# Kernel tuning notes

Hardware: AMD Instinct MI355X
Metric: run time of the kernel (lower is better)

Reference implementation:

```python
import jax, jax.numpy as jnp
import numpy as np

N_ROWS = 4096   # output features (N)
M_COLS = 4096   # input features (M)
BATCH = 4096
NNZ_PER_ROW = 819


def setup_inputs() -> dict:
    rng = np.random.default_rng(0)
    # sample NNZ_PER_ROW distinct, sorted column indices per row (CSR structure)
    cols = np.argsort(rng.random((N_ROWS, M_COLS)), axis=1)[:, :NNZ_PER_ROW]
    cols = np.sort(cols, axis=1).reshape(-1).astype(np.int32)            # [nnz]
    row_ids = np.repeat(np.arange(N_ROWS, dtype=np.int32), NNZ_PER_ROW)  # [nnz], expanded indptr

    key = jax.random.key(0)
    k1, k2, k3 = jax.random.split(key, 3)
    inp = jax.random.normal(k1, (BATCH, M_COLS), dtype=jnp.float32)
    W_val = jax.random.normal(k2, (N_ROWS * NNZ_PER_ROW,), dtype=jnp.float32) * 0.02
    bias = jax.random.normal(k3, (N_ROWS,), dtype=jnp.float32)
    return {
        "input": inp,
        "W_val": W_val,
        "bias": bias,
        "row_ids": jnp.asarray(row_ids),
        "cols": jnp.asarray(cols),
        "N": N_ROWS,
    }


def reference(input, W_val, bias, row_ids, cols, N):
    # Faithful math of SparseLinearFunction: y = x @ W^T + bias where W is the
    # CSR matrix (W_val, row_ids, cols) of shape (N, M). Densify via scatter
    # (CSR has unique (row, col) pairs) then use a single GEMM.
    M = input.shape[-1]
    W = jnp.zeros((N, M), dtype=W_val.dtype).at[row_ids, cols].set(W_val)  # [N, M]
    return jnp.matmul(input, W.T) + bias  # [B, N]
```

## Files before the change

### kernel.cpp

```cpp
#include <hip/hip_runtime.h>
#include <hip/hip_bf16.h>
#include <stdint.h>


#define B_DIM 4096
#define M_DIM 4096
#define N_DIM 4096
#define NNZ_ROW 819
#define BK 32

typedef __attribute__((ext_vector_type(8))) __bf16 bf16x8;
typedef __attribute__((ext_vector_type(4))) float f32x4;

__device__ __forceinline__ unsigned short f32_to_bf16(float f) {
    union { float f; unsigned int u; } v;
    v.f = f;
    unsigned int r = v.u + 0x7FFFu + ((v.u >> 16) & 1u);
    return (unsigned short)(r >> 16);
}

__device__ __forceinline__ void load_lds16(const void* g, void* l) {
    __builtin_amdgcn_global_load_lds(
        (const __attribute__((address_space(1))) void*)g,
        (__attribute__((address_space(3))) void*)l,
        16, 0, 0);
}

__global__ __launch_bounds__(256) void densify_w(
    const float* __restrict__ wval,
    const int* __restrict__ cols,
    unsigned short* __restrict__ wb) {
    __shared__ __attribute__((aligned(16))) unsigned short row_s[M_DIM];
    const int row = blockIdx.x;
    const int tid = threadIdx.x;
    uint4* rs4 = (uint4*)row_s;
    rs4[tid]       = make_uint4(0u, 0u, 0u, 0u);
    rs4[tid + 256] = make_uint4(0u, 0u, 0u, 0u);
    __syncthreads();
    const size_t base = (size_t)row * NNZ_ROW;
    for (int j = tid; j < NNZ_ROW; j += 256) {
        const int c = cols[base + j];
        row_s[c] = f32_to_bf16(wval[base + j]);
    }
    __syncthreads();
    uint4* dst = (uint4*)(wb + (size_t)row * M_DIM);
    dst[tid]       = rs4[tid];
    dst[tid + 256] = rs4[tid + 256];
}

__global__ __launch_bounds__(256) void cvt_x_bf16(
    const float4* __restrict__ x, uint4* __restrict__ y, int n8) {
    int i = blockIdx.x * 256 + threadIdx.x;
    if (i >= n8) return;
    const float4 a = x[2 * i];
    const float4 b = x[2 * i + 1];
    union { ushort ush[8]; uint4 u4; } o;
    o.ush[0] = f32_to_bf16(a.x); o.ush[1] = f32_to_bf16(a.y);
    o.ush[2] = f32_to_bf16(a.z); o.ush[3] = f32_to_bf16(a.w);
    o.ush[4] = f32_to_bf16(b.x); o.ush[5] = f32_to_bf16(b.y);
    o.ush[6] = f32_to_bf16(b.z); o.ush[7] = f32_to_bf16(b.w);
    y[i] = o.u4;
}


__global__ __launch_bounds__(256, 4) void gemm_bt_bias(
    const unsigned short* __restrict__ Xb,
    const unsigned short* __restrict__ Wb,
    const float* __restrict__ bias,
    float* __restrict__ out)
{
    __shared__ __attribute__((aligned(16))) unsigned short As[2 * 128 * BK];
    __shared__ __attribute__((aligned(16))) unsigned short Bs[2 * 128 * BK];

    const int tid    = threadIdx.x;
    const int wid    = tid >> 6;
    const int lane   = tid & 63;
    const int wm     = wid & 1;
    const int wn     = wid >> 1;
    const int lane15 = lane & 15;
    const int laneq  = lane >> 4;

    const int bm0 = blockIdx.y * 128;
    const int bn0 = blockIdx.x * 128;

    const int srow = (lane >> 2);
    const int skof = ((lane & 3) ^ ((lane >> 3) & 3)) * 8;

    const unsigned short* aSrc0 =
        Xb + (size_t)(bm0 + wid * 16 + srow) * M_DIM + skof;
    const unsigned short* aSrc1 = aSrc0 + (size_t)64 * M_DIM;
    const unsigned short* bSrc0 =
        Wb + (size_t)(bn0 + wid * 16 + srow) * M_DIM + skof;
    const unsigned short* bSrc1 = bSrc0 + (size_t)64 * M_DIM;

    const int dOff0 = wid * 512;
    const int dOff1 = (wid + 4) * 512;

    const int slot = (laneq ^ ((lane15 >> 1) & 3)) * 8;
    int aOff[4], bOff[4];
#pragma unroll
    for (int t = 0; t < 4; ++t) {
        aOff[t] = (wm * 64 + t * 16 + lane15) * BK + slot;
        bOff[t] = (wn * 64 + t * 16 + lane15) * BK + slot;
    }

    f32x4 acc[4][4];
#pragma unroll
    for (int i = 0; i < 4; ++i)
#pragma unroll
        for (int j = 0; j < 4; ++j) acc[i][j] = (f32x4)0.0f;

    load_lds16(aSrc0, As + dOff0);
    load_lds16(aSrc1, As + dOff1);
    load_lds16(bSrc0, Bs + dOff0);
    load_lds16(bSrc1, Bs + dOff1);
    __syncthreads();

    int buf = 0;
    for (int kt = 0; kt < M_DIM; kt += BK) {
        const int nbase = (buf ^ 1) * (128 * BK);
        if (kt + BK < M_DIM) {
            load_lds16(aSrc0 + kt + BK, As + nbase + dOff0);
            load_lds16(aSrc1 + kt + BK, As + nbase + dOff1);
            load_lds16(bSrc0 + kt + BK, Bs + nbase + dOff0);
            load_lds16(bSrc1 + kt + BK, Bs + nbase + dOff1);
        }
        const int cbase = buf * (128 * BK);

        bf16x8 af[4], bf[4];
#pragma unroll
        for (int t = 0; t < 4; ++t) {
            af[t] = *((const bf16x8*)(As + cbase + aOff[t]));
            bf[t] = *((const bf16x8*)(Bs + cbase + bOff[t]));
        }
#pragma unroll
        for (int mt = 0; mt < 4; ++mt)
#pragma unroll
            for (int nt = 0; nt < 4; ++nt)
                acc[mt][nt] = __builtin_amdgcn_mfma_f32_16x16x32_bf16(
                    af[mt], bf[nt], acc[mt][nt], 0, 0, 0);

        __syncthreads();
        buf ^= 1;
    }

#pragma unroll
    for (int nt = 0; nt < 4; ++nt) {
        const int col = bn0 + wn * 64 + nt * 16 + lane15;
        const float bv = bias[col];
#pragma unroll
        for (int mt = 0; mt < 4; ++mt) {
            const int row0 = bm0 + wm * 64 + mt * 16 + laneq * 4;
#pragma unroll
            for (int r = 0; r < 4; ++r) {
                out[(size_t)(row0 + r) * N_DIM + col] = acc[mt][nt][r] + bv;
            }
        }
    }
}


extern "C" void kernel_launch(void* const* d_in, const int* in_sizes, int n_in,
                              void* d_out, int out_size, void* d_ws, size_t ws_size,
                              hipStream_t stream) {
    const float* x       = (const float*)d_in[0];
    const float* wval    = (const float*)d_in[1];
    const float* bias    = (const float*)d_in[2];
    const int*   cols    = (const int*)d_in[4];
    float* out = (float*)d_out;

    unsigned short* Wb = (unsigned short*)d_ws;
    unsigned short* Xb = Wb + (size_t)N_DIM * M_DIM;

    densify_w<<<dim3(N_DIM), dim3(256), 0, stream>>>(wval, cols, Wb);
    {
        int n8 = (B_DIM * M_DIM) / 8;
        cvt_x_bf16<<<dim3(n8 / 256), dim3(256), 0, stream>>>(
            (const float4*)x, (uint4*)Xb, n8);
    }
    gemm_bt_bias<<<dim3(N_DIM / 128, B_DIM / 128), dim3(256), 0, stream>>>(
        Xb, Wb, bias, out);
}
```

Before: 296.9 us.

## Rewrite GEMM as 256x256 tile, 8-wave, BK=64 phased pipeline with XCD swizzle

Replaces the 128x128, 4-wave, BK=32 double-buffered GEMM with a 256x256 block tile computed by 8 waves. Each 64-wide K step is split into four quadrant phases that interleave global-to-LDS staging with MFMA work, using a manual vmcnt wait and raw barriers plus setprio around the MFMA clusters. Block indices are also remapped so that neighbouring tiles land on the same XCD for L2 reuse. The aim is more data reuse per LDS load and better overlap of loads with compute. The cost is higher register and LDS use (128KB shared) and hand-tuned wait counts, which are fragile.

```diff
diff --git a/kernel.cpp b/kernel.cpp
--- a/kernel.cpp
+++ b/kernel.cpp
@@ -7,7 +7,6 @@
 #define M_DIM 4096
 #define N_DIM 4096
 #define NNZ_ROW 819
-#define BK 32
 
 typedef __attribute__((ext_vector_type(8))) __bf16 bf16x8;
 typedef __attribute__((ext_vector_type(4))) float f32x4;
@@ -62,101 +61,147 @@
     y[i] = o.u4;
 }
 
-
-__global__ __launch_bounds__(256, 4) void gemm_bt_bias(
+__device__ __forceinline__ void stage_half(
+    const unsigned short* __restrict__ src,
+    int grow0,
+    int kt,
+    unsigned short* dst,
+    int w, int l) {
+#pragma unroll
+    for (int j = 0; j < 2; ++j) {
+        const int seg = w * 2 + j;
+        const int r   = seg * 8 + (l >> 3);
+        const int cg  = (l >> 3) ^ (l & 7);
+        load_lds16(src + (size_t)(grow0 + r) * M_DIM + kt + cg * 8,
+                   dst + seg * 512);
+    }
+}
+
+template <int MA, int NB, int SK>
+__device__ __forceinline__ void phase_op(
+    const unsigned short* As_c, const unsigned short* Bs_c,
+    unsigned short* As_n, unsigned short* Bs_n,
+    const unsigned short* __restrict__ Xb, const unsigned short* __restrict__ Wb,
+    int bm0, int bn0, int kn, bool do_stage,
+    int wr, int wc, int w, int l, f32x4 (&acc)[2][4][2][2]) {
+    const int l15 = l & 15;
+    const int lg  = l >> 4;
+    const int lx  = l & 7;
+    const int ck0 = (lg ^ lx) << 3;
+    const int ck1 = ((4 + lg) ^ lx) << 3;
+
+    const unsigned short* Ab = As_c + (MA * 128 + wr * 64 + l15) * 64;
+    const unsigned short* Bb = Bs_c + (NB * 128 + wc * 32 + l15) * 64;
+
+    bf16x8 af[4][2], bfr[2][2];
+#pragma unroll
+    for (int mf = 0; mf < 4; ++mf) {
+        af[mf][0] = *(const bf16x8*)(Ab + mf * 1024 + ck0);
+        af[mf][1] = *(const bf16x8*)(Ab + mf * 1024 + ck1);
+    }
+#pragma unroll
+    for (int nf = 0; nf < 2; ++nf) {
+        bfr[nf][0] = *(const bf16x8*)(Bb + nf * 1024 + ck0);
+        bfr[nf][1] = *(const bf16x8*)(Bb + nf * 1024 + ck1);
+    }
+
+    if (do_stage) {
+        if constexpr (SK == 0) stage_half(Xb, bm0,       kn, As_n,        w, l);
+        if constexpr (SK == 1) stage_half(Wb, bn0,       kn, Bs_n,        w, l);
+        if constexpr (SK == 2) stage_half(Xb, bm0 + 128, kn, As_n + 8192, w, l);
+        if constexpr (SK == 3) stage_half(Wb, bn0 + 128, kn, Bs_n + 8192, w, l);
+    }
+
+    asm volatile("s_waitcnt vmcnt(4)" ::: "memory");
+    asm volatile("s_barrier" ::: "memory");
+
+    __builtin_amdgcn_s_setprio(1);
+#pragma unroll
+    for (int mf = 0; mf < 4; ++mf)
+#pragma unroll
+        for (int nf = 0; nf < 2; ++nf) {
+            acc[MA][mf][NB][nf] = __builtin_amdgcn_mfma_f32_16x16x32_bf16(
+                af[mf][0], bfr[nf][0], acc[MA][mf][NB][nf], 0, 0, 0);
+            acc[MA][mf][NB][nf] = __builtin_amdgcn_mfma_f32_16x16x32_bf16(
+                af[mf][1], bfr[nf][1], acc[MA][mf][NB][nf], 0, 0, 0);
+        }
+    __builtin_amdgcn_s_setprio(0);
+    asm volatile("s_barrier" ::: "memory");
+}
+
+__global__ __launch_bounds__(512, 2) void gemm_bt_bias(
     const unsigned short* __restrict__ Xb,
     const unsigned short* __restrict__ Wb,
     const float* __restrict__ bias,
     float* __restrict__ out)
 {
-    __shared__ __attribute__((aligned(16))) unsigned short As[2 * 128 * BK];
-    __shared__ __attribute__((aligned(16))) unsigned short Bs[2 * 128 * BK];
-
-    const int tid    = threadIdx.x;
-    const int wid    = tid >> 6;
-    const int lane   = tid & 63;
-    const int wm     = wid & 1;
-    const int wn     = wid >> 1;
-    const int lane15 = lane & 15;
-    const int laneq  = lane >> 4;
-
-    const int bm0 = blockIdx.y * 128;
-    const int bn0 = blockIdx.x * 128;
-
-    const int srow = (lane >> 2);
-    const int skof = ((lane & 3) ^ ((lane >> 3) & 3)) * 8;
-
-    const unsigned short* aSrc0 =
-        Xb + (size_t)(bm0 + wid * 16 + srow) * M_DIM + skof;
-    const unsigned short* aSrc1 = aSrc0 + (size_t)64 * M_DIM;
-    const unsigned short* bSrc0 =
-        Wb + (size_t)(bn0 + wid * 16 + srow) * M_DIM + skof;
-    const unsigned short* bSrc1 = bSrc0 + (size_t)64 * M_DIM;
-
-    const int dOff0 = wid * 512;
-    const int dOff1 = (wid + 4) * 512;
-
-    const int slot = (laneq ^ ((lane15 >> 1) & 3)) * 8;
-    int aOff[4], bOff[4];
-#pragma unroll
-    for (int t = 0; t < 4; ++t) {
-        aOff[t] = (wm * 64 + t * 16 + lane15) * BK + slot;
-        bOff[t] = (wn * 64 + t * 16 + lane15) * BK + slot;
-    }
-
-    f32x4 acc[4][4];
-#pragma unroll
-    for (int i = 0; i < 4; ++i)
-#pragma unroll
-        for (int j = 0; j < 4; ++j) acc[i][j] = (f32x4)0.0f;
-
-    load_lds16(aSrc0, As + dOff0);
-    load_lds16(aSrc1, As + dOff1);
-    load_lds16(bSrc0, Bs + dOff0);
-    load_lds16(bSrc1, Bs + dOff1);
-    __syncthreads();
-
-    int buf = 0;
-    for (int kt = 0; kt < M_DIM; kt += BK) {
-        const int nbase = (buf ^ 1) * (128 * BK);
-        if (kt + BK < M_DIM) {
-            load_lds16(aSrc0 + kt + BK, As + nbase + dOff0);
-            load_lds16(aSrc1 + kt + BK, As + nbase + dOff1);
-            load_lds16(bSrc0 + kt + BK, Bs + nbase + dOff0);
-            load_lds16(bSrc1 + kt + BK, Bs + nbase + dOff1);
+    __shared__ __attribute__((aligned(16))) unsigned short As0[16384];
+    __shared__ __attribute__((aligned(16))) unsigned short Bs0[16384];
+    __shared__ __attribute__((aligned(16))) unsigned short As1[16384];
+    __shared__ __attribute__((aligned(16))) unsigned short Bs1[16384];
+
+    const int tid = threadIdx.x;
+    const int w   = tid >> 6;
+    const int l   = tid & 63;
+    const int wr  = w >> 2;
+    const int wc  = w & 3;
+
+    const int wg  = blockIdx.y * 16 + blockIdx.x;
+    const int idx = ((wg & 7) << 5) | (wg >> 3);
+    const int bm0 = (idx >> 4) * 256;
+    const int bn0 = (idx & 15) * 256;
+
+    f32x4 acc[2][4][2][2];
+#pragma unroll
+    for (int a = 0; a < 2; ++a)
+#pragma unroll
+        for (int b = 0; b < 4; ++b)
+#pragma unroll
+            for (int c = 0; c < 2; ++c)
+#pragma unroll
+                for (int d = 0; d < 2; ++d) acc[a][b][c][d] = (f32x4)0.0f;
+
+    stage_half(Xb, bm0,       0, As0,        w, l);
+    stage_half(Wb, bn0,       0, Bs0,        w, l);
+    stage_half(Xb, bm0 + 128, 0, As0 + 8192, w, l);
+    stage_half(Wb, bn0 + 128, 0, Bs0 + 8192, w, l);
+    asm volatile("s_waitcnt vmcnt(0)" ::: "memory");
+    asm volatile("s_barrier" ::: "memory");
+
+#pragma unroll 1
+    for (int kt = 0; kt < M_DIM; kt += 128) {
+        const int k1 = kt + 64;
+        const int k2 = kt + 128;
+        const bool s2 = (k2 < M_DIM);
+        phase_op<0,0,0>(As0,Bs0, As1,Bs1, Xb,Wb, bm0,bn0, k1, true, wr,wc,w,l, acc);
+        phase_op<1,0,1>(As0,Bs0, As1,Bs1, Xb,Wb, bm0,bn0, k1, true, wr,wc,w,l, acc);
+        phase_op<1,1,2>(As0,Bs0, As1,Bs1, Xb,Wb, bm0,bn0, k1, true, wr,wc,w,l, acc);
+        phase_op<0,1,3>(As0,Bs0, As1,Bs1, Xb,Wb, bm0,bn0, k1, true, wr,wc,w,l, acc);
+        phase_op<0,0,0>(As1,Bs1, As0,Bs0, Xb,Wb, bm0,bn0, k2, s2,   wr,wc,w,l, acc);
+        phase_op<1,0,1>(As1,Bs1, As0,Bs0, Xb,Wb, bm0,bn0, k2, s2,   wr,wc,w,l, acc);
+        phase_op<1,1,2>(As1,Bs1, As0,Bs0, Xb,Wb, bm0,bn0, k2, s2,   wr,wc,w,l, acc);
+        phase_op<0,1,3>(As1,Bs1, As0,Bs0, Xb,Wb, bm0,bn0, k2, s2,   wr,wc,w,l, acc);
+    }
+
+    const int l15 = l & 15;
+    const int lg  = l >> 4;
+#pragma unroll
+    for (int nb = 0; nb < 2; ++nb)
+#pragma unroll
+        for (int nf = 0; nf < 2; ++nf) {
+            const int col = bn0 + nb * 128 + wc * 32 + nf * 16 + l15;
+            const float bv = bias[col];
+#pragma unroll
+            for (int ma = 0; ma < 2; ++ma)
+#pragma unroll
+                for (int mf = 0; mf < 4; ++mf) {
+                    const int row0 = bm0 + ma * 128 + wr * 64 + mf * 16 + lg * 4;
+#pragma unroll
+                    for (int r = 0; r < 4; ++r)
+                        out[(size_t)(row0 + r) * N_DIM + col] =
+                            acc[ma][mf][nb][nf][r] + bv;
+                }
         }
-        const int cbase = buf * (128 * BK);
-
-        bf16x8 af[4], bf[4];
-#pragma unroll
-        for (int t = 0; t < 4; ++t) {
-            af[t] = *((const bf16x8*)(As + cbase + aOff[t]));
-            bf[t] = *((const bf16x8*)(Bs + cbase + bOff[t]));
-        }
-#pragma unroll
-        for (int mt = 0; mt < 4; ++mt)
-#pragma unroll
-            for (int nt = 0; nt < 4; ++nt)
-                acc[mt][nt] = __builtin_amdgcn_mfma_f32_16x16x32_bf16(
-                    af[mt], bf[nt], acc[mt][nt], 0, 0, 0);
-
-        __syncthreads();
-        buf ^= 1;
-    }
-
-#pragma unroll
-    for (int nt = 0; nt < 4; ++nt) {
-        const int col = bn0 + wn * 64 + nt * 16 + lane15;
-        const float bv = bias[col];
-#pragma unroll
-        for (int mt = 0; mt < 4; ++mt) {
-            const int row0 = bm0 + wm * 64 + mt * 16 + laneq * 4;
-#pragma unroll
-            for (int r = 0; r < 4; ++r) {
-                out[(size_t)(row0 + r) * N_DIM + col] = acc[mt][nt][r] + bv;
-            }
-        }
-    }
 }
 
 
@@ -178,6 +223,6 @@
         cvt_x_bf16<<<dim3(n8 / 256), dim3(256), 0, stream>>>(
             (const float4*)x, (uint4*)Xb, n8);
     }
-    gemm_bt_bias<<<dim3(N_DIM / 128, B_DIM / 128), dim3(256), 0, stream>>>(
+    gemm_bt_bias<<<dim3(N_DIM / 256, B_DIM / 256), dim3(512), 0, stream>>>(
         Xb, Wb, bias, out);
 }
```

Result: no change. 298.9 us (+0.7%).
